# Kernel optimization log

Measured on AMD Instinct MI355X. Metric: run time of the kernel, lower is better.

## Reference

```python
import jax, jax.numpy as jnp
import numpy as np

NUM_BINS = 32
SIGMA_RATIO = 0.5          # Gaussian Parzen window width relative to bin spacing
SMOOTH_NR = 1e-07
SMOOTH_DR = 1e-07


def setup_inputs() -> dict:
    key = jax.random.key(0)
    k1, k2 = jax.random.split(key)
    shape = (2, 1, 96, 96, 96)
    pred = jax.random.uniform(k1, shape, dtype=jnp.float32)
    target = jax.random.uniform(k2, shape, dtype=jnp.float32)
    return {"pred": pred, "target": target}


def _parzen_weights(img_flat, bin_centers, preterm):
    # img_flat: [B, N]; bin_centers: [nb]
    # Gaussian Parzen window, normalized so each voxel's weights sum to 1 over bins.
    d = img_flat[..., None] - bin_centers          # [B, N, nb]
    w = jnp.exp(-preterm * d * d)                  # [B, N, nb]
    return w / jnp.sum(w, axis=-1, keepdims=True)


def reference(pred, target):
    B = pred.shape[0]
    nb = NUM_BINS
    bin_centers = jnp.linspace(0.0, 1.0, nb, dtype=jnp.float32)  # [nb]
    bin_width = 1.0 / (nb - 1)
    sigma = SIGMA_RATIO * bin_width
    preterm = jnp.float32(1.0 / (2.0 * sigma * sigma))

    p = pred.reshape(B, -1)    # [B, N]
    t = target.reshape(B, -1)  # [B, N]
    N = p.shape[1]

    wa = _parzen_weights(p, bin_centers, preterm)  # [B, N, nb]
    wb = _parzen_weights(t, bin_centers, preterm)  # [B, N, nb]

    # joint histogram [B, nb, nb] and marginals [B, 1, nb]
    pab = jnp.einsum('bni,bnj->bij', wa, wb) / N
    pa = jnp.mean(wa, axis=1, keepdims=True).transpose(0, 2, 1).transpose(0, 2, 1)  # [B,1,nb]
    pa = jnp.mean(wa, axis=1)[:, None, :]  # [B, 1, nb]
    pb = jnp.mean(wb, axis=1)[:, None, :]  # [B, 1, nb]

    # papb = bmm(pa^T, pb): outer product of marginals -> [B, nb, nb]
    papb = jnp.einsum('bki,bkj->bij', pa, pb)

    mi = jnp.sum(pab * jnp.log((pab + SMOOTH_NR) / (papb + SMOOTH_DR) + SMOOTH_DR),
                 axis=(-1, -2))  # [B]
    return -jnp.mean(mi)
```

## Files before the change

kernel.cpp:

```cpp
#include <hip/hip_runtime.h>
#include <hip/hip_bf16.h>

#define NBINS 32
#define CHUNK 128
#define NROWS 34
#define STR 136
#define TILE_HALVES (NROWS * STR)
#define NTHREADS 256
#define NVOX 884736
#define BPB 768
#define NCHUNKS 9
#define NSLOTS 16

typedef __attribute__((ext_vector_type(8))) _Float16 half8;
typedef __attribute__((ext_vector_type(16))) float f32x16;
typedef __attribute__((ext_vector_type(4))) int i32x4;

__device__ __forceinline__ void compute_w(float x, int& kb, _Float16* wq) {
    float tt = x * 31.0f;
    float kf = rintf(tt);
    int ki = (int)kf;
    float u = tt - kf;
    kb = ki - 3 + (u > 0.0f ? 1 : 0);
    float w[6];
    float s = 0.0f;
#pragma unroll
    for (int o = 0; o < 6; ++o) {
        int b = kb + o;
        float d = tt - (float)b;
        float e = __expf(-2.0f * d * d);
        e = ((unsigned)b < NBINS) ? e : 0.0f;
        w[o] = e;
        s += e;
    }
    float rinv = 1.0f / s;
#pragma unroll
    for (int o = 0; o < 6; ++o) wq[o] = (_Float16)(w[o] * rinv);
}

__device__ __forceinline__ void zero6(_Float16* __restrict__ L, int col, int kb) {
#pragma unroll
    for (int o = 0; o < 6; ++o) {
        int r = min(max(kb + o, -1), 32) + 1;
        L[r * STR + col] = (_Float16)0.0f;
    }
}
__device__ __forceinline__ void scatter6(_Float16* __restrict__ L, int col, int kb,
                                         const _Float16* wq) {
#pragma unroll
    for (int o = 0; o < 6; ++o) {
        int r = min(max(kb + o, -1), 32) + 1;
        L[r * STR + col] = wq[o];
    }
}

__global__ __launch_bounds__(NTHREADS, 6)
void mi_hist_kernel(const float* __restrict__ pred, const float* __restrict__ targ,
                    float* __restrict__ hist ) {
    __shared__ __attribute__((aligned(16))) _Float16 smem[2 * TILE_HALVES];
    _Float16* TA = smem;
    _Float16* TB = smem + TILE_HALVES;

    const int tid = threadIdx.x;
    const int bx = blockIdx.x;
    const int batch = blockIdx.y;
    const int col = tid & 127;
    const bool isB = tid >= 128;
    const float* src = (isB ? targ : pred) + (size_t)batch * NVOX;
    _Float16* T = isB ? TB : TA;

    const int wid = tid >> 6;
    const int lane = tid & 63;
    const int frag = (1 + (lane & 31)) * STR + wid * 32 + 8 * (lane >> 5);

    float xs[NCHUNKS];
#pragma unroll
    for (int c = 0; c < NCHUNKS; ++c)
        xs[c] = src[((size_t)(c * BPB + bx)) * CHUNK + col];

    {
        i32x4 z = {0, 0, 0, 0};
        i32x4* zp = (i32x4*)smem;
#pragma unroll
        for (int i = 0; i < 5; ++i) {
            int idx = i * NTHREADS + tid;
            if (idx < (2 * TILE_HALVES) / 8) zp[idx] = z;
        }
    }

    f32x16 acc;
#pragma unroll
    for (int r = 0; r < 16; ++r) acc[r] = 0.0f;

    int kb_old = 0;

#define DO_MFMA() { \
        _Pragma("unroll") \
        for (int kk = 0; kk < 2; ++kk) { \
            half8 af = *(const half8*)&TA[frag + kk * 16]; \
            half8 bf = *(const half8*)&TB[frag + kk * 16]; \
            acc = __builtin_amdgcn_mfma_f32_32x32x16_f16(af, bf, acc, 0, 0, 0); \
        } }

    {
        _Float16 wq[6]; int kb;
        compute_w(xs[0], kb, wq);
        __syncthreads();
        scatter6(T, col, kb, wq);
        kb_old = kb;
        __syncthreads();
        DO_MFMA();
    }
#pragma unroll
    for (int c = 1; c < NCHUNKS; ++c) {
        _Float16 wq[6]; int kb;
        compute_w(xs[c], kb, wq);
        __syncthreads();
        zero6(T, col, kb_old);
        scatter6(T, col, kb, wq);
        kb_old = kb;
        __syncthreads();
        DO_MFMA();
    }
    __syncthreads();

    float* red = (float*)smem;
    const int colc = lane & 31;
    const int rlo = 4 * (lane >> 5);
#pragma unroll
    for (int r = 0; r < 16; ++r) {
        int rowc = (r & 3) + 8 * (r >> 2) + rlo;
        red[wid * 1024 + rowc * 32 + colc] = acc[r];
    }
    __syncthreads();
    float* H = hist + ((size_t)(bx & (NSLOTS - 1)) * 2 + batch) * 1024;
    for (int idx = tid; idx < 1024; idx += NTHREADS) {
        float s = red[idx] + red[1024 + idx] + red[2048 + idx] + red[3072 + idx];
        atomicAdd(&H[idx], s);
    }
}

__global__ void mi_reduce_kernel(const float* __restrict__ hist, float* __restrict__ out) {
    __shared__ float s_pab[2 * NBINS * NBINS];
    __shared__ double s_pa[2][NBINS];
    __shared__ double s_pb[2][NBINS];
    __shared__ double s_red[1024];
    const int tid = threadIdx.x;
    const double invN = 1.0 / (double)NVOX;

    for (int g = tid; g < 512; g += 1024) {
        float4 s = make_float4(0.f, 0.f, 0.f, 0.f);
        for (int sl = 0; sl < NSLOTS; ++sl) {
            float4 v = ((const float4*)hist)[sl * 512 + g];
            s.x += v.x; s.y += v.y; s.z += v.z; s.w += v.w;
        }
        ((float4*)s_pab)[g] = s;
    }
    __syncthreads();

    if (tid < 64) {
        int b = tid >> 5, i = tid & 31;
        double s = 0.0;
        for (int j = 0; j < NBINS; ++j) s += (double)s_pab[(b * NBINS + i) * NBINS + j];
        s_pa[b][i] = s * invN;
    } else if (tid < 128) {
        int t2 = tid - 64;
        int b = t2 >> 5, j = t2 & 31;
        double s = 0.0;
        for (int i = 0; i < NBINS; ++i) s += (double)s_pab[(b * NBINS + i) * NBINS + j];
        s_pb[b][j] = s * invN;
    }
    __syncthreads();

    double acc = 0.0;
    for (int idx = tid; idx < 2 * NBINS * NBINS; idx += 1024) {
        int b = idx >> 10;
        int cell = idx & 1023;
        int i = cell >> 5, j = cell & 31;
        double pab = (double)s_pab[idx] * invN;
        double papb = s_pa[b][i] * s_pb[b][j];
        acc += pab * log((pab + 1e-7) / (papb + 1e-7) + 1e-7);
    }
    s_red[tid] = acc;
    __syncthreads();
    for (int s2 = 512; s2 > 0; s2 >>= 1) {
        if (tid < s2) s_red[tid] += s_red[tid + s2];
        __syncthreads();
    }
    if (tid == 0) out[0] = (float)(-0.5 * s_red[0]);
}

extern "C" void kernel_launch(void* const* d_in, const int* in_sizes, int n_in,
                              void* d_out, int out_size, void* d_ws, size_t ws_size,
                              hipStream_t stream) {
    const float* pred = (const float*)d_in[0];
    const float* targ = (const float*)d_in[1];
    float* hist = (float*)d_ws;
    float* out = (float*)d_out;

    hipMemsetAsync(hist, 0, NSLOTS * 2 * NBINS * NBINS * sizeof(float), stream);
    dim3 grid(BPB, 2);
    hipLaunchKernelGGL(mi_hist_kernel, grid, dim3(NTHREADS), 0, stream, pred, targ, hist);
    hipLaunchKernelGGL(mi_reduce_kernel, dim3(1), dim3(1024), 0, stream, hist, out);
}
```

Baseline: 30.08 us.

## Warp-specialize histogram kernel into producer/consumer waves with double-buffered LDS

Splits the block into two producer waves that compute Parzen weights and scatter them into double-buffered LDS tiles, and two consumer waves that run MFMA on completed tiles. Hand-off uses LDS flag spin-waits instead of block-wide barriers. Each block now covers 13–14 chunks and the grid shrinks from 768 to 512 blocks, so weight computation can overlap matrix work. The cost is half the waves doing MFMA, spin-wait overhead, fewer blocks, and lower occupancy from the larger shared buffer.

```diff
diff --git a/kernel.cpp b/kernel.cpp
--- a/kernel.cpp
+++ b/kernel.cpp
@@ -6,10 +6,10 @@
 #define NROWS 34
 #define STR 136
 #define TILE_HALVES (NROWS * STR)
+#define BUF_HALVES (2 * TILE_HALVES)
 #define NTHREADS 256
 #define NVOX 884736
-#define BPB 768
-#define NCHUNKS 9
+#define BPB 512
 #define NSLOTS 16
 
 typedef __attribute__((ext_vector_type(8))) _Float16 half8;
@@ -54,89 +54,131 @@
     }
 }
 
-__global__ __launch_bounds__(NTHREADS, 6)
+__device__ __forceinline__ int flg_load(const int* f) {
+    return __hip_atomic_load(f, __ATOMIC_ACQUIRE, __HIP_MEMORY_SCOPE_WORKGROUP);
+}
+__device__ __forceinline__ void flg_store(int* f, int v) {
+    __hip_atomic_store(f, v, __ATOMIC_RELEASE, __HIP_MEMORY_SCOPE_WORKGROUP);
+}
+
+__global__ __launch_bounds__(NTHREADS, 4)
 void mi_hist_kernel(const float* __restrict__ pred, const float* __restrict__ targ,
                     float* __restrict__ hist ) {
-    __shared__ __attribute__((aligned(16))) _Float16 smem[2 * TILE_HALVES];
-    _Float16* TA = smem;
-    _Float16* TB = smem + TILE_HALVES;
+    __shared__ __attribute__((aligned(16))) _Float16 smem[2 * BUF_HALVES];
+    __shared__ int flg[8];
 
     const int tid = threadIdx.x;
     const int bx = blockIdx.x;
     const int batch = blockIdx.y;
-    const int col = tid & 127;
-    const bool isB = tid >= 128;
-    const float* src = (isB ? targ : pred) + (size_t)batch * NVOX;
-    _Float16* T = isB ? TB : TA;
-
     const int wid = tid >> 6;
     const int lane = tid & 63;
-    const int frag = (1 + (lane & 31)) * STR + wid * 32 + 8 * (lane >> 5);
-
-    float xs[NCHUNKS];
-#pragma unroll
-    for (int c = 0; c < NCHUNKS; ++c)
-        xs[c] = src[((size_t)(c * BPB + bx)) * CHUNK + col];
+    const int nchunks = (bx < 256) ? 14 : 13;
 
     {
         i32x4 z = {0, 0, 0, 0};
         i32x4* zp = (i32x4*)smem;
-#pragma unroll
-        for (int i = 0; i < 5; ++i) {
-            int idx = i * NTHREADS + tid;
-            if (idx < (2 * TILE_HALVES) / 8) zp[idx] = z;
-        }
-    }
+        for (int i = tid; i < (2 * BUF_HALVES) / 8; i += NTHREADS) zp[i] = z;
+    }
+    if (tid < 8) flg[tid] = 0;
 
     f32x16 acc;
 #pragma unroll
     for (int r = 0; r < 16; ++r) acc[r] = 0.0f;
 
-    int kb_old = 0;
-
-#define DO_MFMA() { \
+    __syncthreads();
+
+    if (wid < 2) {
+        const float* src = ((wid == 1) ? targ : pred) + (size_t)batch * NVOX;
+        _Float16* T0 = smem + wid * TILE_HALVES;
+        _Float16* T1 = smem + BUF_HALVES + wid * TILE_HALVES;
+        int* myp0 = &flg[0 * 2 + wid];
+        int* myp1 = &flg[1 * 2 + wid];
+        const int c1 = lane, c2 = lane + 64;
+
+        float av = src[(size_t)bx * CHUNK + c1];
+        float bv = src[(size_t)bx * CHUNK + c2];
+        int kA0 = 0, kB0 = 0, kA1 = 0, kB1 = 0;
+
+#define PROD(C, T, MYP, KA, KB, DO_ZERO) { \
+        float an = 0.0f, bn = 0.0f; \
+        if ((C) + 1 < nchunks) { \
+            size_t v = ((size_t)((C) + 1) * BPB + bx) * CHUNK; \
+            an = src[v + c1]; bn = src[v + c2]; \
+        } \
+        if (DO_ZERO) {  \
+            int e = (C) - 1; \
+            while (flg_load(&flg[4 + ((C) & 1) * 2 + 0]) < e) {} \
+            while (flg_load(&flg[4 + ((C) & 1) * 2 + 1]) < e) {} \
+        } \
+        { _Float16 wq[6]; int kb; \
+          compute_w(av, kb, wq); \
+          if (DO_ZERO) zero6(T, c1, KA); \
+          scatter6(T, c1, kb, wq); KA = kb; \
+          compute_w(bv, kb, wq); \
+          if (DO_ZERO) zero6(T, c2, KB); \
+          scatter6(T, c2, kb, wq); KB = kb; } \
+        if (lane == 0) flg_store(MYP, (C) + 1); \
+        av = an; bv = bn; }
+
+        PROD(0, T0, myp0, kA0, kB0, false)
+        PROD(1, T1, myp1, kA1, kB1, false)
+#pragma unroll 1
+        for (int j = 1; j <= 5; ++j) {
+            PROD(2 * j,     T0, myp0, kA0, kB0, true)
+            PROD(2 * j + 1, T1, myp1, kA1, kB1, true)
+        }
+        PROD(12, T0, myp0, kA0, kB0, true)
+        if (nchunks == 14) { PROD(13, T1, myp1, kA1, kB1, true) }
+#undef PROD
+    } else {
+        const int ci = wid - 2;
+        const int frag = (1 + (lane & 31)) * STR + ci * 64 + 8 * (lane >> 5);
+        int* myc0 = &flg[4 + 0 * 2 + ci];
+        int* myc1 = &flg[4 + 1 * 2 + ci];
+
+#define CONS(C, QB, MYC) { \
+        int e = (C) + 1; \
+        while (flg_load(&flg[(QB) * 2 + 0]) < e) {} \
+        while (flg_load(&flg[(QB) * 2 + 1]) < e) {} \
+        const _Float16* PA = smem + (QB) * BUF_HALVES; \
+        const _Float16* PB = PA + TILE_HALVES; \
         _Pragma("unroll") \
-        for (int kk = 0; kk < 2; ++kk) { \
-            half8 af = *(const half8*)&TA[frag + kk * 16]; \
-            half8 bf = *(const half8*)&TB[frag + kk * 16]; \
+        for (int kk = 0; kk < 4; ++kk) { \
+            half8 af = *(const half8*)&PA[frag + kk * 16]; \
+            half8 bf = *(const half8*)&PB[frag + kk * 16]; \
             acc = __builtin_amdgcn_mfma_f32_32x32x16_f16(af, bf, acc, 0, 0, 0); \
-        } }
-
-    {
-        _Float16 wq[6]; int kb;
-        compute_w(xs[0], kb, wq);
-        __syncthreads();
-        scatter6(T, col, kb, wq);
-        kb_old = kb;
-        __syncthreads();
-        DO_MFMA();
-    }
-#pragma unroll
-    for (int c = 1; c < NCHUNKS; ++c) {
-        _Float16 wq[6]; int kb;
-        compute_w(xs[c], kb, wq);
-        __syncthreads();
-        zero6(T, col, kb_old);
-        scatter6(T, col, kb, wq);
-        kb_old = kb;
-        __syncthreads();
-        DO_MFMA();
-    }
+        } \
+        if (lane == 0) flg_store(MYC, e); }
+
+        CONS(0, 0, myc0)
+        CONS(1, 1, myc1)
+#pragma unroll 1
+        for (int j = 1; j <= 5; ++j) {
+            CONS(2 * j,     0, myc0)
+            CONS(2 * j + 1, 1, myc1)
+        }
+        CONS(12, 0, myc0)
+        if (nchunks == 14) { CONS(13, 1, myc1) }
+#undef CONS
+    }
+
     __syncthreads();
 
     float* red = (float*)smem;
-    const int colc = lane & 31;
-    const int rlo = 4 * (lane >> 5);
-#pragma unroll
-    for (int r = 0; r < 16; ++r) {
-        int rowc = (r & 3) + 8 * (r >> 2) + rlo;
-        red[wid * 1024 + rowc * 32 + colc] = acc[r];
+    if (wid >= 2) {
+        const int ci = wid - 2;
+        const int colc = lane & 31;
+        const int rlo = 4 * (lane >> 5);
+#pragma unroll
+        for (int r = 0; r < 16; ++r) {
+            int rowc = (r & 3) + 8 * (r >> 2) + rlo;
+            red[ci * 1024 + rowc * 32 + colc] = acc[r];
+        }
     }
     __syncthreads();
     float* H = hist + ((size_t)(bx & (NSLOTS - 1)) * 2 + batch) * 1024;
     for (int idx = tid; idx < 1024; idx += NTHREADS) {
-        float s = red[idx] + red[1024 + idx] + red[2048 + idx] + red[3072 + idx];
-        atomicAdd(&H[idx], s);
+        atomicAdd(&H[idx], red[idx] + red[1024 + idx]);
     }
 }
 
```

After: 34.83 us. +15.8%, slower.
